# Kernel tuning notes

Measured on AMD Instinct MI355X. Metric: run time of the kernel, lower is better.

The kernel has to match this reference:

```python
import jax, jax.numpy as jnp
import numpy as np

B, S, D_MODEL, NUM_HEADS, DFF = 4, 2048, 256, 8, 1024
DEPTH = D_MODEL // NUM_HEADS
EPS = 1e-6
LENGTH_SCALE = 1.0


def setup_inputs() -> dict:
    key = jax.random.key(0)
    ks = jax.random.split(key, 18)
    n = lambda k, shp, s=0.05: (jax.random.normal(k, shp, dtype=jnp.float32) * s)
    return {
        "x": jax.random.normal(ks[0], (B, S, D_MODEL), dtype=jnp.float32),
        "wq_w": n(ks[1], (D_MODEL, D_MODEL)), "wq_b": jnp.zeros((D_MODEL,), jnp.float32),
        "wk_w": n(ks[2], (D_MODEL, D_MODEL)), "wk_b": jnp.zeros((D_MODEL,), jnp.float32),
        "wv_w": n(ks[3], (D_MODEL, D_MODEL)), "wv_b": jnp.zeros((D_MODEL,), jnp.float32),
        "wo_w": n(ks[4], (D_MODEL, D_MODEL)), "wo_b": jnp.zeros((D_MODEL,), jnp.float32),
        "ffn1_w": n(ks[5], (D_MODEL, DFF)), "ffn1_b": jnp.zeros((DFF,), jnp.float32),
        "ffn2_w": n(ks[6], (DFF, D_MODEL)), "ffn2_b": jnp.zeros((D_MODEL,), jnp.float32),
        "ln1_g": jnp.ones((D_MODEL,), jnp.float32), "ln1_b": jnp.zeros((D_MODEL,), jnp.float32),
        "ln2_g": jnp.ones((D_MODEL,), jnp.float32), "ln2_b": jnp.zeros((D_MODEL,), jnp.float32),
    }


def _layernorm(x, g, b):
    mu = jnp.mean(x, axis=-1, keepdims=True)
    var = jnp.mean(jnp.square(x - mu), axis=-1, keepdims=True)
    return (x - mu) * jax.lax.rsqrt(var + EPS) * g + b


def _split_heads(t):
    # [B,S,D_MODEL] -> [B,H,S,depth]
    return t.reshape(B, S, NUM_HEADS, DEPTH).transpose(0, 2, 1, 3)


def _encoder_layer(x, wq_w, wq_b, wk_w, wk_b, wv_w, wv_b, wo_w, wo_b,
                   ffn1_w, ffn1_b, ffn2_w, ffn2_b, ln1_g, ln1_b, ln2_g, ln2_b):
    q = _split_heads(x @ wq_w + wq_b)
    k = _split_heads(x @ wk_w + wk_b)
    v = _split_heads(x @ wv_w + wv_b)
    # pairwise squared distances: ||q||^2 - 2 q.k + ||k||^2 -> [B,H,S,S]
    q2 = jnp.sum(q * q, axis=-1)  # [B,H,S]
    k2 = jnp.sum(k * k, axis=-1)  # [B,H,S]
    dists = q2[..., :, None] - 2.0 * jnp.einsum("bhqd,bhkd->bhqk", q, k) + k2[..., None, :]
    # exponentiated-quadratic kernel, then softmax over keys (mask=None)
    attn = jax.nn.softmax(jnp.exp(-0.5 * dists / (LENGTH_SCALE ** 2)), axis=-1)
    out = jnp.einsum("bhqk,bhkd->bhqd", attn, v)  # [B,H,S,depth]
    out = out.transpose(0, 2, 1, 3).reshape(B, S, D_MODEL)
    attn_out = out @ wo_w + wo_b
    # dropout is identity (training=False)
    out1 = _layernorm(x + attn_out, ln1_g, ln1_b)
    ffn = jax.nn.relu(out1 @ ffn1_w + ffn1_b) @ ffn2_w + ffn2_b
    return _layernorm(out1 + ffn, ln2_g, ln2_b)


def reference(x, wq_w, wq_b, wk_w, wk_b, wv_w, wv_b, wo_w, wo_b,
              ffn1_w, ffn1_b, ffn2_w, ffn2_b, ln1_g, ln1_b, ln2_g, ln2_b):
    return _encoder_layer(x, wq_w, wq_b, wk_w, wk_b, wv_w, wv_b, wo_w, wo_b,
                          ffn1_w, ffn1_b, ffn2_w, ffn2_b, ln1_g, ln1_b, ln2_g, ln2_b)
```

## Files before the change

kernel.cpp:

```cpp
#include <hip/hip_runtime.h>
#include <hip/hip_bf16.h>

#define SQL  2048
#define DM   256
#define LNEPS 1e-6f
#define LOG2E    (1.44269504f)

#define B_XB    (0ull)
#define B_QB    (4ull<<20)
#define B_KB    (8ull<<20)
#define B_VT    (12ull<<20)
#define B_CTX   (16ull<<20)
#define B_O1B   (20ull<<20)
#define B_O1F   (24ull<<20)
#define B_MID   (32ull<<20)
#define B_WQKVT (48ull<<20)
#define B_WOT   ((48ull<<20)+(512ull<<10))
#define B_W1T   (49ull<<20)
#define B_W2T   ((49ull<<20)+(512ull<<10))
#define B_BQKV  (50ull<<20)
#define B_HQ    ((50ull<<20)+(64ull<<10))
#define B_HK    ((50ull<<20)+(320ull<<10))
#define B_C2    (0ull)

typedef float  f32x16 __attribute__((ext_vector_type(16)));
typedef short  bf16x8 __attribute__((ext_vector_type(8)));
typedef int    i32x4  __attribute__((ext_vector_type(4)));
typedef int    i32x2  __attribute__((ext_vector_type(2)));

static __device__ __forceinline__ unsigned short bfu(float f){
    __hip_bfloat16 h = __float2bfloat16(f);
    return *reinterpret_cast<unsigned short*>(&h);
}
static __device__ __forceinline__ unsigned pk2(float a, float b){
    return (unsigned)bfu(a) | ((unsigned)bfu(b) << 16);
}
static __device__ __forceinline__ void glds16(const void* g, void* l){
    __builtin_amdgcn_global_load_lds((const __attribute__((address_space(1))) unsigned int*)g,
                                     (__attribute__((address_space(3))) unsigned int*)l, 16, 0, 0);
}

__global__ __launch_bounds__(256) void k_packall(
    const float* __restrict__ wq, const float* __restrict__ wk, const float* __restrict__ wv,
    const float* __restrict__ wo, const float* __restrict__ w1, const float* __restrict__ w2,
    const float* __restrict__ bq, const float* __restrict__ bk, const float* __restrict__ bv,
    const float* __restrict__ x,
    unsigned short* __restrict__ wqkvT, unsigned short* __restrict__ woT,
    unsigned short* __restrict__ w1T, unsigned short* __restrict__ w2T,
    float* __restrict__ bqkv, unsigned short* __restrict__ xb)
{
    __shared__ float tile[32][33];
    const int bid = blockIdx.x;
    const int t = threadIdx.x;
    if (bid < 768) {
        const float* W; unsigned short* Wt; int K, N, xk, yn;
        if (bid < 192) {
            int which = bid >> 6, local = bid & 63;
            W = (which == 0) ? wq : (which == 1 ? wk : wv);
            Wt = wqkvT + which * 65536; K = 256; N = 256;
            xk = local & 7; yn = local >> 3;
        } else if (bid < 256) {
            int local = bid - 192; W = wo; Wt = woT; K = 256; N = 256;
            xk = local & 7; yn = local >> 3;
        } else if (bid < 512) {
            int local = bid - 256; W = w1; Wt = w1T; K = 256; N = 1024;
            xk = local & 7; yn = local >> 3;
        } else {
            int local = bid - 512; W = w2; Wt = w2T; K = 1024; N = 256;
            xk = local & 31; yn = local >> 5;
        }
        const int tx = t & 31, ty = t >> 5;
        const int kb = xk * 32, nb = yn * 32;
#pragma unroll
        for (int i = 0; i < 32; i += 8) tile[ty + i][tx] = W[(size_t)(kb + ty + i) * N + nb + tx];
        __syncthreads();
#pragma unroll
        for (int i = 0; i < 32; i += 8) Wt[(size_t)(nb + ty + i) * K + kb + tx] = bfu(tile[tx][ty + i]);
    } else if (bid < 771) {
        int wb = bid - 768;
        const float* s = (wb == 0) ? bq : (wb == 1 ? bk : bv);
        bqkv[wb * 256 + t] = s[t];
    } else {
        const int i = (bid - 771) * 256 + t;
        float4 v = ((const float4*)x)[i];
        ushort4 o; o.x = bfu(v.x); o.y = bfu(v.y); o.z = bfu(v.z); o.w = bfu(v.w);
        ((ushort4*)xb)[i] = o;
    }
}

__global__ __launch_bounds__(256, 2) void k_qkv(
    const unsigned short* __restrict__ A, const unsigned short* __restrict__ Bt,
    const float* __restrict__ bias,
    unsigned short* __restrict__ qb, unsigned short* __restrict__ kb,
    char* __restrict__ vtg)
{
    __shared__ __align__(16) char smem[65536];
    const int t = threadIdx.x;
    const int lane = t & 63, w = t >> 6;
    const int lo = lane & 31, hi = lane >> 5;
    const int row0 = blockIdx.x * 128;
    const int col0 = blockIdx.y * 128;
    f32x16 acc[2][2] = {};
    const int gS = lane & 7;
    const int rr = w * 32 + (lane >> 3);

    auto stage = [&](int buf, int kt) {
        const int k0 = kt * 64;
        char* As = smem + buf * 32768;
        char* Bs = As + 16384;
#pragma unroll
        for (int i = 0; i < 4; ++i) {
            const int r = rr + i * 8;
            glds16((const char*)(A  + (size_t)(row0 + r) * 256 + k0) + ((gS ^ (r & 7)) << 4),
                   As + w * 4096 + i * 1024 + lane * 16);
            glds16((const char*)(Bt + (size_t)(col0 + r) * 256 + k0) + ((gS ^ (r & 7)) << 4),
                   Bs + w * 4096 + i * 1024 + lane * 16);
        }
    };

    stage(0, 0);
    __syncthreads();
    for (int kt = 0; kt < 4; ++kt) {
        if (kt + 1 < 4) stage((kt + 1) & 1, kt + 1);
        const char* As = smem + (kt & 1) * 32768;
        const char* Bs = As + 16384;
        const int rA = (w >> 1) * 64 + lo;
        const int rB = (w & 1) * 64 + lo;
#pragma unroll
        for (int s = 0; s < 4; ++s) {
            const int g = s * 2 + hi;
            bf16x8 fa0 = *(const bf16x8*)(As + rA * 128 + ((g ^ (rA & 7)) << 4));
            bf16x8 fa1 = *(const bf16x8*)(As + (rA + 32) * 128 + ((g ^ (rA & 7)) << 4));
            bf16x8 fb0 = *(const bf16x8*)(Bs + rB * 128 + ((g ^ (rB & 7)) << 4));
            bf16x8 fb1 = *(const bf16x8*)(Bs + (rB + 32) * 128 + ((g ^ (rB & 7)) << 4));
            acc[0][0] = __builtin_amdgcn_mfma_f32_32x32x16_bf16(fa0, fb0, acc[0][0], 0, 0, 0);
            acc[0][1] = __builtin_amdgcn_mfma_f32_32x32x16_bf16(fa0, fb1, acc[0][1], 0, 0, 0);
            acc[1][0] = __builtin_amdgcn_mfma_f32_32x32x16_bf16(fa1, fb0, acc[1][0], 0, 0, 0);
            acc[1][1] = __builtin_amdgcn_mfma_f32_32x32x16_bf16(fa1, fb1, acc[1][1], 0, 0, 0);
        }
        __syncthreads();
    }
#pragma unroll
    for (int m = 0; m < 2; ++m)
#pragma unroll
    for (int n = 0; n < 2; ++n) {
        const int c0 = col0 + (w & 1) * 64 + n * 32;
        const int which = c0 >> 8, h = (c0 >> 5) & 7;
        const float bv = bias[c0 + lo];
        if (which < 2) {
            unsigned short* dst = (which == 0) ? qb : kb;
            const float scl = (which == 0) ? LOG2E : 1.0f;
#pragma unroll
            for (int r = 0; r < 16; ++r) {
                const int gr = row0 + (w >> 1) * 64 + m * 32 + (r & 3) + 8 * (r >> 2) + 4 * hi;
                const int b = gr >> 11, s = gr & 2047;
                dst[(((size_t)(b * 8 + h)) * SQL + s) * 32 + lo] = bfu((acc[m][n][r] + bv) * scl);
            }
        } else {
#pragma unroll
            for (int r = 0; r < 16; ++r) {
                const int gr = row0 + (w >> 1) * 64 + m * 32 + (r & 3) + 8 * (r >> 2) + 4 * hi;
                const int b = gr >> 11, s = gr & 2047;
                const int o = s * 2;
                const int op = (o & ~0x78) | ((((o >> 3) & 15) ^ (lo & 15)) << 3);
                *(unsigned short*)(vtg + ((size_t)(b * 8 + h)) * 131072 + (size_t)lo * 4096 + op)
                    = bfu(acc[m][n][r] + bv);
            }
        }
    }
}

__global__ __launch_bounds__(256) void k_h2(const unsigned short* __restrict__ qb,
                                            const unsigned short* __restrict__ kb,
                                            unsigned int* __restrict__ hqp,
                                            unsigned int* __restrict__ hkp)
{
    const int gid = blockIdx.x * 256 + threadIdx.x;
    const unsigned short* qp = qb + (size_t)gid * 32;
    const unsigned short* kp = kb + (size_t)gid * 32;
    float sq = 0.f, sk = 0.f;
#pragma unroll
    for (int i = 0; i < 4; ++i) {
        i32x4 qv = *(const i32x4*)(qp + i * 8);
        i32x4 kv = *(const i32x4*)(kp + i * 8);
#pragma unroll
        for (int j = 0; j < 4; ++j) {
            unsigned int qw = (unsigned int)qv[j], kw = (unsigned int)kv[j];
            float a = __builtin_bit_cast(float, qw << 16);
            float c = __builtin_bit_cast(float, qw & 0xffff0000u);
            float d = __builtin_bit_cast(float, kw << 16);
            float e = __builtin_bit_cast(float, kw & 0xffff0000u);
            sq += a * a + c * c; sk += d * d + e * e;
        }
    }
    const float hq = -0.34657359f * sq + 0.52876637f;
    const float hk = -0.72134752f * sk;
    hqp[gid] = 0x3F80u | ((unsigned)bfu(hq) << 16);
    hkp[gid] = (unsigned)bfu(hk) | 0x3F800000u;
}

__global__ __launch_bounds__(512, 4) void k_attn(
    const unsigned short* __restrict__ qg, const unsigned short* __restrict__ kg,
    const char* __restrict__ vtg, const unsigned int* __restrict__ hqp,
    const unsigned int* __restrict__ hkp, unsigned short* __restrict__ ctxb)
{
    __shared__ __align__(16) char smem[34048];
    char* kls = smem;
    char* vtl = smem + 16384;
    float* hks  = (float*)(smem + 32768);
    float* invs = (float*)(smem + 33792);
    float* redacc = (float*)smem;
    float* redden = (float*)(smem + 24576);

    const int t = threadIdx.x;
    const int grp = t >> 7;
    const int tl  = t & 127;
    const int lane = t & 63;
    const int w   = (t >> 6) & 1;
    const int lo = lane & 31;
    const int hi = lane >> 5;

    const int bid = (blockIdx.x & 7) * 128 + (blockIdx.x >> 3);
    const int qc = bid & 31;
    const int bh = bid >> 5;

    const int qrow = qc * 64 + w * 32 + lo;
    const unsigned short* qp = qg + ((size_t)bh * SQL + qrow) * 32;
    const bf16x8 qf0 = *(const bf16x8*)(qp + hi * 8);
    const bf16x8 qf1 = *(const bf16x8*)(qp + 16 + hi * 8);
    i32x4 b3i = {};
    if (hi == 0) b3i[0] = (int)hqp[(size_t)bh * SQL + qrow];
    const bf16x8 b3 = __builtin_bit_cast(bf16x8, b3i);

    f32x16 acc = {};
    float den = 0.f;

    const unsigned short* kbg = kg + (size_t)bh * SQL * 32;
    const char* vtb = vtg + (size_t)bh * 131072;
    const unsigned int* hkb = hkp + (size_t)bh * SQL;
    char* kd = kls + grp * 4096;
    char* vd = vtl + grp * 4096;

    for (int kt = 0; kt < 8; ++kt) {
        const int key0 = grp * 512 + kt * 64;
        {
#pragma unroll
            for (int it = 0; it < 2; ++it) {
                const int idx = it * 128 + tl;
                const int r = idx >> 2, gl = idx & 3;
                glds16((const char*)(kbg + (size_t)(key0 + r) * 32) + ((gl ^ ((r >> 1) & 3)) << 4),
                       kd + idx * 16);
                const int vrw = idx >> 3, vch = idx & 7;
                glds16(vtb + (size_t)vrw * 4096 + key0 * 2 + vch * 16, vd + idx * 16);
            }
            if (tl < 64) hks[grp * 64 + tl] = __builtin_bit_cast(float, hkb[key0 + tl]);
        }
        __syncthreads();

#pragma unroll
        for (int h2 = 0; h2 < 2; ++h2) {
            const int kb32 = h2 * 32;
            const int kA = kb32 + lo;
            const char* krow = kd + kA * 64;
            const int ksw = (kA >> 1) & 3;
            bf16x8 kf0 = *(const bf16x8*)(krow + (((0 + hi) ^ ksw) << 4));
            bf16x8 kf1 = *(const bf16x8*)(krow + (((2 + hi) ^ ksw) << 4));
            i32x4 a3i = {};
            if (hi == 0) a3i[0] = __builtin_bit_cast(int, hks[grp * 64 + kA]);
            f32x16 sc = {};
            __builtin_amdgcn_s_setprio(1);
            sc = __builtin_amdgcn_mfma_f32_32x32x16_bf16(kf0, qf0, sc, 0, 0, 0);
            sc = __builtin_amdgcn_mfma_f32_32x32x16_bf16(kf1, qf1, sc, 0, 0, 0);
            sc = __builtin_amdgcn_mfma_f32_32x32x16_bf16(
                     __builtin_bit_cast(bf16x8, a3i), b3, sc, 0, 0, 0);
            __builtin_amdgcn_s_setprio(0);
            float wv[16];
#pragma unroll
            for (int r = 0; r < 16; ++r) {
                float e1 = __builtin_amdgcn_exp2f(sc[r]);
                float ww = __builtin_amdgcn_exp2f(e1);
                den += ww;
                wv[r] = ww;
            }
            i32x4 p0; p0[0]=pk2(wv[0],wv[1]);   p0[1]=pk2(wv[2],wv[3]);
                      p0[2]=pk2(wv[4],wv[5]);   p0[3]=pk2(wv[6],wv[7]);
            i32x4 p1; p1[0]=pk2(wv[8],wv[9]);   p1[1]=pk2(wv[10],wv[11]);
                      p1[2]=pk2(wv[12],wv[13]); p1[3]=pk2(wv[14],wv[15]);
            const char* vrow = vd + lo * 128;
            const int vxor = (lo & 15) << 3;
            const int o0 = (kb32 + 4 * hi) * 2;
            const int o1 = (kb32 + 16 + 4 * hi) * 2;
            i32x2 a0 = *(const i32x2*)(vrow + (o0 ^ vxor));
            i32x2 a1 = *(const i32x2*)(vrow + ((o0 + 16) ^ vxor));
            i32x2 b0 = *(const i32x2*)(vrow + (o1 ^ vxor));
            i32x2 b1 = *(const i32x2*)(vrow + ((o1 + 16) ^ vxor));
            i32x4 vb0; vb0[0]=a0[0]; vb0[1]=a0[1]; vb0[2]=a1[0]; vb0[3]=a1[1];
            i32x4 vb1; vb1[0]=b0[0]; vb1[1]=b0[1]; vb1[2]=b1[0]; vb1[3]=b1[1];
            __builtin_amdgcn_s_setprio(1);
            acc = __builtin_amdgcn_mfma_f32_32x32x16_bf16(
                __builtin_bit_cast(bf16x8, p0), __builtin_bit_cast(bf16x8, vb0), acc, 0, 0, 0);
            acc = __builtin_amdgcn_mfma_f32_32x32x16_bf16(
                __builtin_bit_cast(bf16x8, p1), __builtin_bit_cast(bf16x8, vb1), acc, 0, 0, 0);
            __builtin_amdgcn_s_setprio(0);
        }
        __syncthreads();
    }

    if (grp != 0) {
#pragma unroll
        for (int r = 0; r < 16; ++r) redacc[((grp - 1) * 16 + r) * 128 + tl] = acc[r];
        redden[(grp - 1) * 128 + tl] = den;
    }
    __syncthreads();
    if (grp == 0) {
#pragma unroll
        for (int r = 0; r < 16; ++r)
            acc[r] += redacc[r * 128 + tl] + redacc[(16 + r) * 128 + tl] + redacc[(32 + r) * 128 + tl];
        den += redden[tl] + redden[128 + tl] + redden[256 + tl];
        const float dfull = den + __shfl_xor(den, 32);
        if (hi == 0) invs[w * 32 + lo] = 1.f / dfull;
        float4 i0 = *(const float4*)&invs[w * 32 + 4 * hi];
        float4 i1 = *(const float4*)&invs[w * 32 + 8 + 4 * hi];
        float4 i2 = *(const float4*)&invs[w * 32 + 16 + 4 * hi];
        float4 i3 = *(const float4*)&invs[w * 32 + 24 + 4 * hi];
        float iv[16] = {i0.x,i0.y,i0.z,i0.w, i1.x,i1.y,i1.z,i1.w,
                        i2.x,i2.y,i2.z,i2.w, i3.x,i3.y,i3.z,i3.w};
        const int b = bh >> 3, h = bh & 7;
        unsigned short* cbase = ctxb + ((size_t)(b * SQL + qc * 64 + w * 32)) * 256 + h * 32 + lo;
#pragma unroll
        for (int r = 0; r < 16; ++r) {
            const int qr = (r & 3) + 8 * (r >> 2) + 4 * hi;
            cbase[(size_t)qr * 256] = bfu(acc[r] * iv[r]);
        }
    }
}

template<int KSTRIDE, int KT, int NFULL, int RELU, int OUTF, int OUTB>
__global__ __launch_bounds__(256, 2) void k_gemm(
    const unsigned short* __restrict__ A, const unsigned short* __restrict__ Bt,
    const float* __restrict__ bias,
    float* __restrict__ outf, unsigned short* __restrict__ outb)
{
    __shared__ __align__(16) char smem[65536];
    const int t = threadIdx.x;
    const int lane = t & 63, w = t >> 6;
    const int lo = lane & 31, hi = lane >> 5;
    const int row0 = blockIdx.x * 128;
    const int col0 = blockIdx.y * 128;
    const int z = blockIdx.z;
    f32x16 acc[2][2] = {};
    const int gS = lane & 7;
    const int rr = w * 32 + (lane >> 3);

    auto stage = [&](int buf, int kt) {
        const int k0 = (z * KT + kt) * 64;
        char* As = smem + buf * 32768;
        char* Bs = As + 16384;
#pragma unroll
        for (int i = 0; i < 4; ++i) {
            const int r = rr + i * 8;
            glds16((const char*)(A  + (size_t)(row0 + r) * KSTRIDE + k0) + ((gS ^ (r & 7)) << 4),
                   As + w * 4096 + i * 1024 + lane * 16);
            glds16((const char*)(Bt + (size_t)(col0 + r) * KSTRIDE + k0) + ((gS ^ (r & 7)) << 4),
                   Bs + w * 4096 + i * 1024 + lane * 16);
        }
    };

    stage(0, 0);
    __syncthreads();
    for (int kt = 0; kt < KT; ++kt) {
        if (kt + 1 < KT) stage((kt + 1) & 1, kt + 1);
        const char* As = smem + (kt & 1) * 32768;
        const char* Bs = As + 16384;
        const int rA = (w >> 1) * 64 + lo;
        const int rB = (w & 1) * 64 + lo;
#pragma unroll
        for (int s = 0; s < 4; ++s) {
            const int g = s * 2 + hi;
            bf16x8 fa0 = *(const bf16x8*)(As + rA * 128 + ((g ^ (rA & 7)) << 4));
            bf16x8 fa1 = *(const bf16x8*)(As + (rA + 32) * 128 + ((g ^ (rA & 7)) << 4));
            bf16x8 fb0 = *(const bf16x8*)(Bs + rB * 128 + ((g ^ (rB & 7)) << 4));
            bf16x8 fb1 = *(const bf16x8*)(Bs + (rB + 32) * 128 + ((g ^ (rB & 7)) << 4));
            acc[0][0] = __builtin_amdgcn_mfma_f32_32x32x16_bf16(fa0, fb0, acc[0][0], 0, 0, 0);
            acc[0][1] = __builtin_amdgcn_mfma_f32_32x32x16_bf16(fa0, fb1, acc[0][1], 0, 0, 0);
            acc[1][0] = __builtin_amdgcn_mfma_f32_32x32x16_bf16(fa1, fb0, acc[1][0], 0, 0, 0);
            acc[1][1] = __builtin_amdgcn_mfma_f32_32x32x16_bf16(fa1, fb1, acc[1][1], 0, 0, 0);
        }
        __syncthreads();
    }
#pragma unroll
    for (int m = 0; m < 2; ++m)
#pragma unroll
    for (int n = 0; n < 2; ++n) {
        const int c0 = col0 + (w & 1) * 64 + n * 32;
        const float bv = (z == 0) ? bias[c0 + lo] : 0.f;
#pragma unroll
        for (int r = 0; r < 16; ++r) {
            const int gr = row0 + (w >> 1) * 64 + m * 32 + (r & 3) + 8 * (r >> 2) + 4 * hi;
            float vv = acc[m][n][r] + bv;
            if (RELU) vv = fmaxf(vv, 0.f);
            if (OUTF) outf[(size_t)z * 8192 * NFULL + (size_t)gr * NFULL + c0 + lo] = vv;
            if (OUTB) outb[(size_t)gr * NFULL + c0 + lo] = bfu(vv);
        }
    }
}

template<int DUAL>
__global__ __launch_bounds__(256) void k_lnsum(
    const float* __restrict__ pa, const float* __restrict__ pb,
    const float* __restrict__ res, const float* __restrict__ g,
    const float* __restrict__ bt, float* __restrict__ outf,
    unsigned short* __restrict__ outb)
{
    const int row = blockIdx.x * 4 + (threadIdx.x >> 6);
    const int lane = threadIdx.x & 63;
    const size_t base = (size_t)row * 256;
    float4 v  = ((const float4*)(pa + base))[lane];
    float4 v2 = ((const float4*)(pb + base))[lane];
    float4 v3 = ((const float4*)(res + base))[lane];
    v.x += v2.x + v3.x; v.y += v2.y + v3.y; v.z += v2.z + v3.z; v.w += v2.w + v3.w;
    float s  = v.x + v.y + v.z + v.w;
    float ss = v.x * v.x + v.y * v.y + v.z * v.z + v.w * v.w;
#pragma unroll
    for (int off = 32; off; off >>= 1) { s += __shfl_xor(s, off); ss += __shfl_xor(ss, off); }
    const float mu = s * (1.f / 256.f);
    const float rstd = rsqrtf(ss * (1.f / 256.f) - mu * mu + LNEPS);
    const float4 gg = ((const float4*)g)[lane];
    const float4 bb = ((const float4*)bt)[lane];
    float4 o;
    o.x = (v.x - mu) * rstd * gg.x + bb.x;
    o.y = (v.y - mu) * rstd * gg.y + bb.y;
    o.z = (v.z - mu) * rstd * gg.z + bb.z;
    o.w = (v.w - mu) * rstd * gg.w + bb.w;
    ((float4*)(outf + base))[lane] = o;
    if (DUAL) {
        ushort4 ob; ob.x = bfu(o.x); ob.y = bfu(o.y); ob.z = bfu(o.z); ob.w = bfu(o.w);
        ((ushort4*)(outb + base))[lane] = ob;
    }
}

extern "C" void kernel_launch(void* const* d_in, const int* in_sizes, int n_in,
                              void* d_out, int out_size, void* d_ws, size_t ws_size,
                              hipStream_t stream) {
    const float* x   = (const float*)d_in[0];
    const float* wq  = (const float*)d_in[1];  const float* bq  = (const float*)d_in[2];
    const float* wk  = (const float*)d_in[3];  const float* bk  = (const float*)d_in[4];
    const float* wv  = (const float*)d_in[5];  const float* bv  = (const float*)d_in[6];
    const float* wo  = (const float*)d_in[7];  const float* wob = (const float*)d_in[8];
    const float* w1  = (const float*)d_in[9];  const float* b1  = (const float*)d_in[10];
    const float* w2  = (const float*)d_in[11]; const float* b2  = (const float*)d_in[12];
    const float* g1  = (const float*)d_in[13]; const float* bl1 = (const float*)d_in[14];
    const float* g2  = (const float*)d_in[15]; const float* bl2 = (const float*)d_in[16];

    char* ws = (char*)d_ws;
    unsigned short* xb    = (unsigned short*)(ws + B_XB);
    unsigned short* qb    = (unsigned short*)(ws + B_QB);
    unsigned short* kbuf  = (unsigned short*)(ws + B_KB);
    char*           vt    = (char*)(ws + B_VT);
    unsigned short* ctxb  = (unsigned short*)(ws + B_CTX);
    unsigned short* o1b   = (unsigned short*)(ws + B_O1B);
    float*          o1f   = (float*)(ws + B_O1F);
    unsigned short* mid   = (unsigned short*)(ws + B_MID);
    float*          c1    = (float*)(ws + B_MID);
    float*          c2    = (float*)(ws + B_C2);
    unsigned short* wqkvT = (unsigned short*)(ws + B_WQKVT);
    unsigned short* woT   = (unsigned short*)(ws + B_WOT);
    unsigned short* w1T   = (unsigned short*)(ws + B_W1T);
    unsigned short* w2T   = (unsigned short*)(ws + B_W2T);
    float* bqkv = (float*)(ws + B_BQKV);
    unsigned int* hqp = (unsigned int*)(ws + B_HQ);
    unsigned int* hkp = (unsigned int*)(ws + B_HK);
    float* out  = (float*)d_out;

    k_packall<<<dim3(2819), dim3(256), 0, stream>>>(wq, wk, wv, wo, w1, w2, bq, bk, bv, x,
                                                    wqkvT, woT, w1T, w2T, bqkv, xb);
    k_qkv<<<dim3(64, 6), dim3(256), 0, stream>>>(xb, wqkvT, bqkv, qb, kbuf, vt);
    k_h2<<<dim3(256), dim3(256), 0, stream>>>(qb, kbuf, hqp, hkp);
    k_attn<<<dim3(1024), dim3(512), 0, stream>>>(qb, kbuf, vt, hqp, hkp, ctxb);
    k_gemm<256, 2, 256, 0, 1, 0><<<dim3(64, 2, 2), dim3(256), 0, stream>>>(ctxb, woT, wob, c1, nullptr);
    k_lnsum<1><<<dim3(2048), dim3(256), 0, stream>>>(c1, c1 + 2097152, x, g1, bl1, o1f, o1b);
    k_gemm<256, 4, 1024, 1, 0, 1><<<dim3(64, 8, 1), dim3(256), 0, stream>>>(o1b, w1T, b1, nullptr, mid);
    k_gemm<1024, 8, 256, 0, 1, 0><<<dim3(64, 2, 2), dim3(256), 0, stream>>>(mid, w2T, b2, c2, nullptr);
    k_lnsum<0><<<dim3(2048), dim3(256), 0, stream>>>(c2, c2 + 2097152, o1f, g2, bl2, out, nullptr);
}
```

Measured before the change: 192.0 us.

## Shrink GEMM tiles, drop split-K and double buffering, fuse norms into QKV

The GEMM and QKV kernels now use 64x128 tiles with single-buffered shared memory (24KB) instead of 128x128 double-buffered tiles (64KB). This roughly doubles the block count and raises the occupancy target. Split-K in the output and FFN2 projections is removed, so the layernorm kernels read one partial sum instead of two. The separate k_h2 kernel is gone: the QKV epilogue computes the squared norms of q and k with wave shuffles, which saves a launch and a re-read of q and k. The trade-off is that the load of the next K slice no longer overlaps with MFMA work, and the epilogue gains many shuffle reductions.

```diff
diff --git a/kernel.cpp b/kernel.cpp
--- a/kernel.cpp
+++ b/kernel.cpp
@@ -88,63 +88,56 @@
     }
 }
 
-__global__ __launch_bounds__(256, 2) void k_qkv(
+__global__ __launch_bounds__(256, 4) void k_qkv(
     const unsigned short* __restrict__ A, const unsigned short* __restrict__ Bt,
     const float* __restrict__ bias,
     unsigned short* __restrict__ qb, unsigned short* __restrict__ kb,
-    char* __restrict__ vtg)
+    char* __restrict__ vtg,
+    unsigned int* __restrict__ hqp, unsigned int* __restrict__ hkp)
 {
-    __shared__ __align__(16) char smem[65536];
+    __shared__ __align__(16) char As[8192];
+    __shared__ __align__(16) char Bs[16384];
     const int t = threadIdx.x;
     const int lane = t & 63, w = t >> 6;
     const int lo = lane & 31, hi = lane >> 5;
-    const int row0 = blockIdx.x * 128;
+    const int row0 = blockIdx.x * 64;
     const int col0 = blockIdx.y * 128;
-    f32x16 acc[2][2] = {};
-    const int gS = lane & 7;
-    const int rr = w * 32 + (lane >> 3);
-
-    auto stage = [&](int buf, int kt) {
+    const int mr = (w & 1) * 32, nc = (w >> 1) * 64;
+    f32x16 acc[2] = {};
+
+    for (int kt = 0; kt < 4; ++kt) {
         const int k0 = kt * 64;
-        char* As = smem + buf * 32768;
-        char* Bs = As + 16384;
-#pragma unroll
-        for (int i = 0; i < 4; ++i) {
-            const int r = rr + i * 8;
-            glds16((const char*)(A  + (size_t)(row0 + r) * 256 + k0) + ((gS ^ (r & 7)) << 4),
-                   As + w * 4096 + i * 1024 + lane * 16);
-            glds16((const char*)(Bt + (size_t)(col0 + r) * 256 + k0) + ((gS ^ (r & 7)) << 4),
-                   Bs + w * 4096 + i * 1024 + lane * 16);
-        }
-    };
-
-    stage(0, 0);
-    __syncthreads();
-    for (int kt = 0; kt < 4; ++kt) {
-        if (kt + 1 < 4) stage((kt + 1) & 1, kt + 1);
-        const char* As = smem + (kt & 1) * 32768;
-        const char* Bs = As + 16384;
-        const int rA = (w >> 1) * 64 + lo;
-        const int rB = (w & 1) * 64 + lo;
+#pragma unroll
+        for (int it = 0; it < 2; ++it) {
+            const int idx = it * 256 + t;
+            const int r = idx >> 3, g = idx & 7;
+            glds16((const char*)(A + (size_t)(row0 + r) * 256 + k0) + ((g ^ (r & 7)) << 4),
+                   As + it * 4096 + w * 1024 + lane * 16);
+        }
+#pragma unroll
+        for (int it = 0; it < 4; ++it) {
+            const int idx = it * 256 + t;
+            const int r = idx >> 3, g = idx & 7;
+            glds16((const char*)(Bt + (size_t)(col0 + r) * 256 + k0) + ((g ^ (r & 7)) << 4),
+                   Bs + it * 4096 + w * 1024 + lane * 16);
+        }
+        __syncthreads();
+        const int rA = mr + lo;
+        const int rB = nc + lo;
 #pragma unroll
         for (int s = 0; s < 4; ++s) {
             const int g = s * 2 + hi;
-            bf16x8 fa0 = *(const bf16x8*)(As + rA * 128 + ((g ^ (rA & 7)) << 4));
-            bf16x8 fa1 = *(const bf16x8*)(As + (rA + 32) * 128 + ((g ^ (rA & 7)) << 4));
+            bf16x8 fa  = *(const bf16x8*)(As + rA * 128 + ((g ^ (rA & 7)) << 4));
             bf16x8 fb0 = *(const bf16x8*)(Bs + rB * 128 + ((g ^ (rB & 7)) << 4));
             bf16x8 fb1 = *(const bf16x8*)(Bs + (rB + 32) * 128 + ((g ^ (rB & 7)) << 4));
-            acc[0][0] = __builtin_amdgcn_mfma_f32_32x32x16_bf16(fa0, fb0, acc[0][0], 0, 0, 0);
-            acc[0][1] = __builtin_amdgcn_mfma_f32_32x32x16_bf16(fa0, fb1, acc[0][1], 0, 0, 0);
-            acc[1][0] = __builtin_amdgcn_mfma_f32_32x32x16_bf16(fa1, fb0, acc[1][0], 0, 0, 0);
-            acc[1][1] = __builtin_amdgcn_mfma_f32_32x32x16_bf16(fa1, fb1, acc[1][1], 0, 0, 0);
-        }
-        __syncthreads();
-    }
-#pragma unroll
-    for (int m = 0; m < 2; ++m)
+            acc[0] = __builtin_amdgcn_mfma_f32_32x32x16_bf16(fa, fb0, acc[0], 0, 0, 0);
+            acc[1] = __builtin_amdgcn_mfma_f32_32x32x16_bf16(fa, fb1, acc[1], 0, 0, 0);
+        }
+        __syncthreads();
+    }
 #pragma unroll
     for (int n = 0; n < 2; ++n) {
-        const int c0 = col0 + (w & 1) * 64 + n * 32;
+        const int c0 = col0 + nc + n * 32;
         const int which = c0 >> 8, h = (c0 >> 5) & 7;
         const float bv = bias[c0 + lo];
         if (which < 2) {
@@ -152,51 +145,35 @@
             const float scl = (which == 0) ? LOG2E : 1.0f;
 #pragma unroll
             for (int r = 0; r < 16; ++r) {
-                const int gr = row0 + (w >> 1) * 64 + m * 32 + (r & 3) + 8 * (r >> 2) + 4 * hi;
+                const int gr = row0 + mr + (r & 3) + 8 * (r >> 2) + 4 * hi;
                 const int b = gr >> 11, s = gr & 2047;
-                dst[(((size_t)(b * 8 + h)) * SQL + s) * 32 + lo] = bfu((acc[m][n][r] + bv) * scl);
+                const unsigned short u = bfu((acc[n][r] + bv) * scl);
+                dst[(((size_t)(b * 8 + h)) * SQL + s) * 32 + lo] = u;
+                const float vr = __builtin_bit_cast(float, ((unsigned)u) << 16);
+                float sv = vr * vr;
+                sv += __shfl_xor(sv, 1);  sv += __shfl_xor(sv, 2);
+                sv += __shfl_xor(sv, 4);  sv += __shfl_xor(sv, 8);
+                sv += __shfl_xor(sv, 16);
+                if (lo == 0) {
+                    const size_t gi = (size_t)(b * 8 + h) * SQL + s;
+                    if (which == 0)
+                        hqp[gi] = 0x3F80u | ((unsigned)bfu(-0.34657359f * sv + 0.52876637f) << 16);
+                    else
+                        hkp[gi] = (unsigned)bfu(-0.72134752f * sv) | 0x3F800000u;
+                }
             }
         } else {
 #pragma unroll
             for (int r = 0; r < 16; ++r) {
-                const int gr = row0 + (w >> 1) * 64 + m * 32 + (r & 3) + 8 * (r >> 2) + 4 * hi;
+                const int gr = row0 + mr + (r & 3) + 8 * (r >> 2) + 4 * hi;
                 const int b = gr >> 11, s = gr & 2047;
                 const int o = s * 2;
                 const int op = (o & ~0x78) | ((((o >> 3) & 15) ^ (lo & 15)) << 3);
                 *(unsigned short*)(vtg + ((size_t)(b * 8 + h)) * 131072 + (size_t)lo * 4096 + op)
-                    = bfu(acc[m][n][r] + bv);
+                    = bfu(acc[n][r] + bv);
             }
         }
     }
-}
-
-__global__ __launch_bounds__(256) void k_h2(const unsigned short* __restrict__ qb,
-                                            const unsigned short* __restrict__ kb,
-                                            unsigned int* __restrict__ hqp,
-                                            unsigned int* __restrict__ hkp)
-{
-    const int gid = blockIdx.x * 256 + threadIdx.x;
-    const unsigned short* qp = qb + (size_t)gid * 32;
-    const unsigned short* kp = kb + (size_t)gid * 32;
-    float sq = 0.f, sk = 0.f;
-#pragma unroll
-    for (int i = 0; i < 4; ++i) {
-        i32x4 qv = *(const i32x4*)(qp + i * 8);
-        i32x4 kv = *(const i32x4*)(kp + i * 8);
-#pragma unroll
-        for (int j = 0; j < 4; ++j) {
-            unsigned int qw = (unsigned int)qv[j], kw = (unsigned int)kv[j];
-            float a = __builtin_bit_cast(float, qw << 16);
-            float c = __builtin_bit_cast(float, qw & 0xffff0000u);
-            float d = __builtin_bit_cast(float, kw << 16);
-            float e = __builtin_bit_cast(float, kw & 0xffff0000u);
-            sq += a * a + c * c; sk += d * d + e * e;
-        }
-    }
-    const float hq = -0.34657359f * sq + 0.52876637f;
-    const float hk = -0.72134752f * sk;
-    hqp[gid] = 0x3F80u | ((unsigned)bfu(hq) << 16);
-    hkp[gid] = (unsigned)bfu(hk) | 0x3F800000u;
 }
 
 __global__ __launch_bounds__(512, 4) void k_attn(
@@ -336,70 +313,61 @@
 }
 
 template<int KSTRIDE, int KT, int NFULL, int RELU, int OUTF, int OUTB>
-__global__ __launch_bounds__(256, 2) void k_gemm(
+__global__ __launch_bounds__(256, 6) void k_gemm(
     const unsigned short* __restrict__ A, const unsigned short* __restrict__ Bt,
     const float* __restrict__ bias,
     float* __restrict__ outf, unsigned short* __restrict__ outb)
 {
-    __shared__ __align__(16) char smem[65536];
+    __shared__ __align__(16) char As[8192];
+    __shared__ __align__(16) char Bs[16384];
     const int t = threadIdx.x;
     const int lane = t & 63, w = t >> 6;
     const int lo = lane & 31, hi = lane >> 5;
-    const int row0 = blockIdx.x * 128;
+    const int row0 = blockIdx.x * 64;
     const int col0 = blockIdx.y * 128;
-    const int z = blockIdx.z;
-    f32x16 acc[2][2] = {};
-    const int gS = lane & 7;
-    const int rr = w * 32 + (lane >> 3);
-
-    auto stage = [&](int buf, int kt) {
-        const int k0 = (z * KT + kt) * 64;
-        char* As = smem + buf * 32768;
-        char* Bs = As + 16384;
-#pragma unroll
-        for (int i = 0; i < 4; ++i) {
-            const int r = rr + i * 8;
-            glds16((const char*)(A  + (size_t)(row0 + r) * KSTRIDE + k0) + ((gS ^ (r & 7)) << 4),
-                   As + w * 4096 + i * 1024 + lane * 16);
-            glds16((const char*)(Bt + (size_t)(col0 + r) * KSTRIDE + k0) + ((gS ^ (r & 7)) << 4),
-                   Bs + w * 4096 + i * 1024 + lane * 16);
-        }
-    };
-
-    stage(0, 0);
-    __syncthreads();
+    const int mr = (w & 1) * 32, nc = (w >> 1) * 64;
+    f32x16 acc[2] = {};
+
     for (int kt = 0; kt < KT; ++kt) {
-        if (kt + 1 < KT) stage((kt + 1) & 1, kt + 1);
-        const char* As = smem + (kt & 1) * 32768;
-        const char* Bs = As + 16384;
-        const int rA = (w >> 1) * 64 + lo;
-        const int rB = (w & 1) * 64 + lo;
+        const int k0 = kt * 64;
+#pragma unroll
+        for (int it = 0; it < 2; ++it) {
+            const int idx = it * 256 + t;
+            const int r = idx >> 3, g = idx & 7;
+            glds16((const char*)(A + (size_t)(row0 + r) * KSTRIDE + k0) + ((g ^ (r & 7)) << 4),
+                   As + it * 4096 + w * 1024 + lane * 16);
+        }
+#pragma unroll
+        for (int it = 0; it < 4; ++it) {
+            const int idx = it * 256 + t;
+            const int r = idx >> 3, g = idx & 7;
+            glds16((const char*)(Bt + (size_t)(col0 + r) * KSTRIDE + k0) + ((g ^ (r & 7)) << 4),
+                   Bs + it * 4096 + w * 1024 + lane * 16);
+        }
+        __syncthreads();
+        const int rA = mr + lo;
+        const int rB = nc + lo;
 #pragma unroll
         for (int s = 0; s < 4; ++s) {
             const int g = s * 2 + hi;
-            bf16x8 fa0 = *(const bf16x8*)(As + rA * 128 + ((g ^ (rA & 7)) << 4));
-            bf16x8 fa1 = *(const bf16x8*)(As + (rA + 32) * 128 + ((g ^ (rA & 7)) << 4));
+            bf16x8 fa  = *(const bf16x8*)(As + rA * 128 + ((g ^ (rA & 7)) << 4));
             bf16x8 fb0 = *(const bf16x8*)(Bs + rB * 128 + ((g ^ (rB & 7)) << 4));
             bf16x8 fb1 = *(const bf16x8*)(Bs + (rB + 32) * 128 + ((g ^ (rB & 7)) << 4));
-            acc[0][0] = __builtin_amdgcn_mfma_f32_32x32x16_bf16(fa0, fb0, acc[0][0], 0, 0, 0);
-            acc[0][1] = __builtin_amdgcn_mfma_f32_32x32x16_bf16(fa0, fb1, acc[0][1], 0, 0, 0);
-            acc[1][0] = __builtin_amdgcn_mfma_f32_32x32x16_bf16(fa1, fb0, acc[1][0], 0, 0, 0);
-            acc[1][1] = __builtin_amdgcn_mfma_f32_32x32x16_bf16(fa1, fb1, acc[1][1], 0, 0, 0);
-        }
-        __syncthreads();
-    }
-#pragma unroll
-    for (int m = 0; m < 2; ++m)
+            acc[0] = __builtin_amdgcn_mfma_f32_32x32x16_bf16(fa, fb0, acc[0], 0, 0, 0);
+            acc[1] = __builtin_amdgcn_mfma_f32_32x32x16_bf16(fa, fb1, acc[1], 0, 0, 0);
+        }
+        __syncthreads();
+    }
 #pragma unroll
     for (int n = 0; n < 2; ++n) {
-        const int c0 = col0 + (w & 1) * 64 + n * 32;
-        const float bv = (z == 0) ? bias[c0 + lo] : 0.f;
+        const int c0 = col0 + nc + n * 32;
+        const float bv = bias[c0 + lo];
 #pragma unroll
         for (int r = 0; r < 16; ++r) {
-            const int gr = row0 + (w >> 1) * 64 + m * 32 + (r & 3) + 8 * (r >> 2) + 4 * hi;
-            float vv = acc[m][n][r] + bv;
+            const int gr = row0 + mr + (r & 3) + 8 * (r >> 2) + 4 * hi;
+            float vv = acc[n][r] + bv;
             if (RELU) vv = fmaxf(vv, 0.f);
-            if (OUTF) outf[(size_t)z * 8192 * NFULL + (size_t)gr * NFULL + c0 + lo] = vv;
+            if (OUTF) outf[(size_t)gr * NFULL + c0 + lo] = vv;
             if (OUTB) outb[(size_t)gr * NFULL + c0 + lo] = bfu(vv);
         }
     }
@@ -407,18 +375,16 @@
 
 template<int DUAL>
 __global__ __launch_bounds__(256) void k_lnsum(
-    const float* __restrict__ pa, const float* __restrict__ pb,
-    const float* __restrict__ res, const float* __restrict__ g,
-    const float* __restrict__ bt, float* __restrict__ outf,
-    unsigned short* __restrict__ outb)
+    const float* __restrict__ pa, const float* __restrict__ res,
+    const float* __restrict__ g, const float* __restrict__ bt,
+    float* __restrict__ outf, unsigned short* __restrict__ outb)
 {
     const int row = blockIdx.x * 4 + (threadIdx.x >> 6);
     const int lane = threadIdx.x & 63;
     const size_t base = (size_t)row * 256;
     float4 v  = ((const float4*)(pa + base))[lane];
-    float4 v2 = ((const float4*)(pb + base))[lane];
     float4 v3 = ((const float4*)(res + base))[lane];
-    v.x += v2.x + v3.x; v.y += v2.y + v3.y; v.z += v2.z + v3.z; v.w += v2.w + v3.w;
+    v.x += v3.x; v.y += v3.y; v.z += v3.z; v.w += v3.w;
     float s  = v.x + v.y + v.z + v.w;
     float ss = v.x * v.x + v.y * v.y + v.z * v.z + v.w * v.w;
 #pragma unroll
@@ -474,12 +440,11 @@
 
     k_packall<<<dim3(2819), dim3(256), 0, stream>>>(wq, wk, wv, wo, w1, w2, bq, bk, bv, x,
                                                     wqkvT, woT, w1T, w2T, bqkv, xb);
-    k_qkv<<<dim3(64, 6), dim3(256), 0, stream>>>(xb, wqkvT, bqkv, qb, kbuf, vt);
-    k_h2<<<dim3(256), dim3(256), 0, stream>>>(qb, kbuf, hqp, hkp);
+    k_qkv<<<dim3(128, 6), dim3(256), 0, stream>>>(xb, wqkvT, bqkv, qb, kbuf, vt, hqp, hkp);
     k_attn<<<dim3(1024), dim3(512), 0, stream>>>(qb, kbuf, vt, hqp, hkp, ctxb);
-    k_gemm<256, 2, 256, 0, 1, 0><<<dim3(64, 2, 2), dim3(256), 0, stream>>>(ctxb, woT, wob, c1, nullptr);
-    k_lnsum<1><<<dim3(2048), dim3(256), 0, stream>>>(c1, c1 + 2097152, x, g1, bl1, o1f, o1b);
-    k_gemm<256, 4, 1024, 1, 0, 1><<<dim3(64, 8, 1), dim3(256), 0, stream>>>(o1b, w1T, b1, nullptr, mid);
-    k_gemm<1024, 8, 256, 0, 1, 0><<<dim3(64, 2, 2), dim3(256), 0, stream>>>(mid, w2T, b2, c2, nullptr);
-    k_lnsum<0><<<dim3(2048), dim3(256), 0, stream>>>(c2, c2 + 2097152, o1f, g2, bl2, out, nullptr);
-}
+    k_gemm<256, 4, 256, 0, 1, 0><<<dim3(128, 2), dim3(256), 0, stream>>>(ctxb, woT, wob, c1, nullptr);
+    k_lnsum<1><<<dim3(2048), dim3(256), 0, stream>>>(c1, x, g1, bl1, o1f, o1b);
+    k_gemm<256, 4, 1024, 1, 0, 1><<<dim3(128, 8), dim3(256), 0, stream>>>(o1b, w1T, b1, nullptr, mid);
+    k_gemm<1024, 16, 256, 0, 1, 0><<<dim3(128, 2), dim3(256), 0, stream>>>(mid, w2T, b2, c2, nullptr);
+    k_lnsum<0><<<dim3(2048), dim3(256), 0, stream>>>(c2, o1f, g2, bl2, out, nullptr);
+}
```

Result: no change. 191.1 us (-0.5%).
